# Kernel tuning notes

Measured on AMD Instinct MI355X. Metric: run time of the kernel, lower is better.

## Reference

```python
import jax, jax.numpy as jnp
import numpy as np
from functools import partial

BETA = 0.5
THR = 1.0
NUM_STEPS = 25

@jax.custom_vjp
def spike_fn(x):
    # Heaviside spike; surrogate gradient (snntorch ATan, alpha=2) in bwd.
    return (x > 0).astype(x.dtype)

def _spike_fwd(x):
    return spike_fn(x), x

def _spike_bwd(x, g):
    return (g / (1.0 + (jnp.pi * x) ** 2),)

spike_fn.defvjp(_spike_fwd, _spike_bwd)

def setup_inputs() -> dict:
    key = jax.random.key(0)
    ks = jax.random.split(key, 12)
    B, I, H, O = 16384, 1024, 1024, 10
    s = 0.05
    return {
        "x":   jax.random.normal(ks[0], (B, I), jnp.float32),
        "W1":  jax.random.normal(ks[1], (H, I), jnp.float32) * s,
        "b1":  jax.random.normal(ks[2], (H,), jnp.float32) * s,
        "V1w": jax.random.normal(ks[3], (H, H), jnp.float32) * s,
        "V1b": jax.random.normal(ks[4], (H,), jnp.float32) * s,
        "W2":  jax.random.normal(ks[5], (H, H), jnp.float32) * s,
        "b2":  jax.random.normal(ks[6], (H,), jnp.float32) * s,
        "V2w": jax.random.normal(ks[7], (H, H), jnp.float32) * s,
        "V2b": jax.random.normal(ks[8], (H,), jnp.float32) * s,
        "W3":  jax.random.normal(ks[9], (O, H), jnp.float32) * s,
        "b3":  jax.random.normal(ks[10], (O,), jnp.float32) * s,
    }

def reference(x, W1, b1, V1w, V1b, W2, b2, V2w, V2b, W3, b3):
    B = x.shape[0]
    H = W1.shape[0]
    cur1 = x @ W1.T + b1  # loop-invariant: fc1(x) recomputed identically each step

    def step(carry, _):
        spk1, mem1, spk2, mem2, ssum = carry
        # RLeaky layer 1: soft reset based on previous mem, recurrent linear on prev spikes
        reset1 = (mem1 > THR).astype(mem1.dtype)
        mem1 = BETA * mem1 + cur1 + spk1 @ V1w.T + V1b - reset1 * THR
        spk1 = spike_fn(mem1 - THR)
        cur2 = spk1 @ W2.T + b2
        reset2 = (mem2 > THR).astype(mem2.dtype)
        mem2 = BETA * mem2 + cur2 + spk2 @ V2w.T + V2b - reset2 * THR
        spk2 = spike_fn(mem2 - THR)
        return (spk1, mem1, spk2, mem2, ssum + spk2), None

    z = jnp.zeros((B, H), x.dtype)
    init = (z, z, z, z, z)
    (s1, m1, s2, m2, spk_sum), _ = jax.lax.scan(step, init, None, length=NUM_STEPS)
    return (spk_sum / NUM_STEPS) @ W3.T + b3
```

## Files before the change

### kernel.cpp

```cpp
#include <hip/hip_runtime.h>


#pragma clang fp contract(off)

#define HDIM 1024
#define SPB (HDIM / 8)
#define BATCH 16384
#define NSTEP 25
#define BMR 128
#define BNC 64
#define BK 32
#define NKT (HDIM / BK)
#define KC 512

__device__ __forceinline__ void stage_a_f32(const float* __restrict__ g, float* s,
                                            int tid, int kt) {
  int row = tid & 127, c = tid >> 7;
  const float* src = g + (size_t)row * HDIM + kt * BK + c * 16;
  float4 v0 = *(const float4*)(src);
  float4 v1 = *(const float4*)(src + 4);
  float4 v2 = *(const float4*)(src + 8);
  float4 v3 = *(const float4*)(src + 12);
  int k0 = c * 16;
  s[(k0 + 0) * BMR + row] = v0.x;  s[(k0 + 1) * BMR + row] = v0.y;
  s[(k0 + 2) * BMR + row] = v0.z;  s[(k0 + 3) * BMR + row] = v0.w;
  s[(k0 + 4) * BMR + row] = v1.x;  s[(k0 + 5) * BMR + row] = v1.y;
  s[(k0 + 6) * BMR + row] = v1.z;  s[(k0 + 7) * BMR + row] = v1.w;
  s[(k0 + 8) * BMR + row] = v2.x;  s[(k0 + 9) * BMR + row] = v2.y;
  s[(k0 + 10) * BMR + row] = v2.z; s[(k0 + 11) * BMR + row] = v2.w;
  s[(k0 + 12) * BMR + row] = v3.x; s[(k0 + 13) * BMR + row] = v3.y;
  s[(k0 + 14) * BMR + row] = v3.z; s[(k0 + 15) * BMR + row] = v3.w;
}

__device__ __forceinline__ void stage_a_u1(const unsigned char* __restrict__ g, float* s,
                                           int tid, int kt) {
  int row = tid & 127, c = tid >> 7;
  unsigned short v =
      *(const unsigned short*)(g + (size_t)row * SPB + kt * 4 + c * 2);
  int k0 = c * 16;
#pragma unroll
  for (int q = 0; q < 16; ++q)
    s[(k0 + q) * BMR + row] = (float)((v >> q) & 1u);
}

__device__ __forceinline__ void stage_b(const float* __restrict__ g, float* s,
                                        int tid, int kt) {
  int row = tid & 63, c = tid >> 6;
  const float* src = g + (size_t)row * HDIM + kt * BK + c * 8;
  float4 v0 = *(const float4*)(src);
  float4 v1 = *(const float4*)(src + 4);
  int k0 = c * 8;
  s[(k0 + 0) * BNC + row] = v0.x; s[(k0 + 1) * BNC + row] = v0.y;
  s[(k0 + 2) * BNC + row] = v0.z; s[(k0 + 3) * BNC + row] = v0.w;
  s[(k0 + 4) * BNC + row] = v1.x; s[(k0 + 5) * BNC + row] = v1.y;
  s[(k0 + 6) * BNC + row] = v1.z; s[(k0 + 7) * BNC + row] = v1.w;
}

template <bool AU1>
__device__ __forceinline__ void kpass(const void* __restrict__ Ag,
                                      const float* __restrict__ Bg,
                                      float* sA, float* sB, int tid, int m0, int n0,
                                      float csum[4][8]) {
  float p[4][8];
#pragma unroll
  for (int m = 0; m < 4; ++m)
#pragma unroll
    for (int n = 0; n < 8; ++n) { csum[m][n] = 0.0f; p[m][n] = 0.0f; }

#pragma unroll 1
  for (int kt = 0; kt < NKT; ++kt) {
    if (AU1) stage_a_u1((const unsigned char*)Ag, sA, tid, kt);
    else     stage_a_f32((const float*)Ag, sA, tid, kt);
    stage_b(Bg, sB, tid, kt);
    __syncthreads();
#pragma unroll
    for (int k = 0; k < BK; ++k) {
      float a[4], b[8];
      *(float4*)&a[0] = *(const float4*)&sA[k * BMR + m0];
      *(float4*)&b[0] = *(const float4*)&sB[k * BNC + n0];
      *(float4*)&b[4] = *(const float4*)&sB[k * BNC + n0 + 4];
#pragma unroll
      for (int m = 0; m < 4; ++m)
#pragma unroll
        for (int n = 0; n < 8; ++n)
          p[m][n] = __builtin_fmaf(a[m], b[n], p[m][n]);
    }
    if (((kt + 1) * BK) % KC == 0) {
#pragma unroll
      for (int m = 0; m < 4; ++m)
#pragma unroll
        for (int n = 0; n < 8; ++n) { csum[m][n] = csum[m][n] + p[m][n]; p[m][n] = 0.0f; }
    }
    __syncthreads();
  }
}

__global__ __launch_bounds__(256) void gemm_cur(const float* __restrict__ A,
                                                const float* __restrict__ B,
                                                const float* __restrict__ bias,
                                                float* __restrict__ outv) {
  __shared__ float sA[BK * BMR];
  __shared__ float sB[BK * BNC];
  const int tid = threadIdx.x;
  const int m0 = (tid >> 3) * 4, n0 = (tid & 7) * 8;
  const int bm = blockIdx.y, bn = blockIdx.x;
  float csum[4][8];
  kpass<false>(A + (size_t)bm * BMR * HDIM, B + (size_t)bn * BNC * HDIM,
               sA, sB, tid, m0, n0, csum);
  const int colb = bn * BNC + n0;
  float4 bia0 = *(const float4*)&bias[colb];
  float4 bia1 = *(const float4*)&bias[colb + 4];
  const float bi[8] = {bia0.x, bia0.y, bia0.z, bia0.w, bia1.x, bia1.y, bia1.z, bia1.w};
#pragma unroll
  for (int m = 0; m < 4; ++m) {
    size_t idx = (size_t)(bm * BMR + m0 + m) * HDIM + colb;
    float o[8];
#pragma unroll
    for (int n = 0; n < 8; ++n) o[n] = csum[m][n] + bi[n];
    *(float4*)&outv[idx] = *(float4*)&o[0];
    *(float4*)&outv[idx + 4] = *(float4*)&o[4];
  }
}

__global__ __launch_bounds__(256) void l1_t0(const float* __restrict__ cur1,
                                             const float* __restrict__ vb,
                                             float* __restrict__ memv,
                                             unsigned char* __restrict__ spk_out) {
  size_t i = ((size_t)blockIdx.x * 256 + threadIdx.x) * 8;
  int col = (int)(i & (HDIM - 1));
  size_t row = i >> 10;
  float au[8], tn[8];
  *(float4*)&au[0] = *(const float4*)&cur1[i];
  *(float4*)&au[4] = *(const float4*)&cur1[i + 4];
  float4 v0 = *(const float4*)&vb[col];
  float4 v1 = *(const float4*)&vb[col + 4];
  const float vbv[8] = {v0.x, v0.y, v0.z, v0.w, v1.x, v1.y, v1.z, v1.w};
  unsigned int bits = 0;
#pragma unroll
  for (int n = 0; n < 8; ++n) {
    float t = 0.5f * 0.0f;
    t = t + au[n];
    t = t + 0.0f;
    t = t + vbv[n];
    t = t - 0.0f;
    tn[n] = t;
    bits |= (((t - 1.0f) > 0.0f) ? 1u : 0u) << n;
  }
  *(float4*)&memv[i] = *(float4*)&tn[0];
  *(float4*)&memv[i + 4] = *(float4*)&tn[4];
  spk_out[row * SPB + (col >> 3)] = (unsigned char)bits;
}

__global__ __launch_bounds__(256) void gemm_l1(
    const unsigned char* __restrict__ A, const float* __restrict__ B,
    const float* __restrict__ vb, const float* __restrict__ cur1,
    float* __restrict__ memv, unsigned char* __restrict__ spk_out) {
  __shared__ float sA[BK * BMR];
  __shared__ float sB[BK * BNC];
  const int tid = threadIdx.x;
  const int m0 = (tid >> 3) * 4, n0 = (tid & 7) * 8;
  const int bm = blockIdx.y, bn = blockIdx.x;
  float csum[4][8];
  kpass<true>(A + (size_t)bm * BMR * SPB, B + (size_t)bn * BNC * HDIM,
              sA, sB, tid, m0, n0, csum);
  const int colb = bn * BNC + n0;
  float4 v0 = *(const float4*)&vb[colb];
  float4 v1 = *(const float4*)&vb[colb + 4];
  const float vbv[8] = {v0.x, v0.y, v0.z, v0.w, v1.x, v1.y, v1.z, v1.w};
#pragma unroll
  for (int m = 0; m < 4; ++m) {
    size_t row = (size_t)(bm * BMR + m0 + m);
    size_t idx = row * HDIM + colb;
    float mo[8], au[8], tn[8];
    *(float4*)&mo[0] = *(const float4*)&memv[idx];
    *(float4*)&mo[4] = *(const float4*)&memv[idx + 4];
    *(float4*)&au[0] = *(const float4*)&cur1[idx];
    *(float4*)&au[4] = *(const float4*)&cur1[idx + 4];
    unsigned int bits = 0;
#pragma unroll
    for (int n = 0; n < 8; ++n) {
      float reset = (mo[n] > 1.0f) ? 1.0f : 0.0f;
      float t = 0.5f * mo[n];
      t = t + au[n];
      t = t + csum[m][n];
      t = t + vbv[n];
      t = t - reset;
      tn[n] = t;
      bits |= (((t - 1.0f) > 0.0f) ? 1u : 0u) << n;
    }
    *(float4*)&memv[idx] = *(float4*)&tn[0];
    *(float4*)&memv[idx + 4] = *(float4*)&tn[4];
    spk_out[row * SPB + (colb >> 3)] = (unsigned char)bits;
  }
}

__global__ __launch_bounds__(256) void gemm_l2f(
    const unsigned char* __restrict__ A1, const float* __restrict__ B1,
    const unsigned char* __restrict__ A2, const float* __restrict__ B2,
    const float* __restrict__ bias, const float* __restrict__ vb,
    float* __restrict__ memv, unsigned char* __restrict__ spk_out,
    unsigned char* __restrict__ ssum, int skip2) {
  __shared__ float sA[BK * BMR];
  __shared__ float sB[BK * BNC];
  const int tid = threadIdx.x;
  const int m0 = (tid >> 3) * 4, n0 = (tid & 7) * 8;
  const int bm = blockIdx.y, bn = blockIdx.x;
  float dot1[4][8], csum[4][8];
  kpass<true>(A1 + (size_t)bm * BMR * SPB, B1 + (size_t)bn * BNC * HDIM,
              sA, sB, tid, m0, n0, dot1);
  if (skip2) {
#pragma unroll
    for (int m = 0; m < 4; ++m)
#pragma unroll
      for (int n = 0; n < 8; ++n) csum[m][n] = 0.0f;
  } else {
    __syncthreads();
    kpass<true>(A2 + (size_t)bm * BMR * SPB, B2 + (size_t)bn * BNC * HDIM,
                sA, sB, tid, m0, n0, csum);
  }
  const int colb = bn * BNC + n0;
  float4 b0 = *(const float4*)&bias[colb];
  float4 b1v = *(const float4*)&bias[colb + 4];
  const float bi[8] = {b0.x, b0.y, b0.z, b0.w, b1v.x, b1v.y, b1v.z, b1v.w};
  float4 v0 = *(const float4*)&vb[colb];
  float4 v1 = *(const float4*)&vb[colb + 4];
  const float vbv[8] = {v0.x, v0.y, v0.z, v0.w, v1.x, v1.y, v1.z, v1.w};
#pragma unroll
  for (int m = 0; m < 4; ++m) {
    size_t row = (size_t)(bm * BMR + m0 + m);
    size_t idx = row * HDIM + colb;
    float mo[8], tn[8];
    *(float4*)&mo[0] = *(const float4*)&memv[idx];
    *(float4*)&mo[4] = *(const float4*)&memv[idx + 4];
    unsigned int bits = 0;
#pragma unroll
    for (int n = 0; n < 8; ++n) {
      float reset = (mo[n] > 1.0f) ? 1.0f : 0.0f;
      float cur2 = dot1[m][n] + bi[n];
      float t = 0.5f * mo[n];
      t = t + cur2;
      t = t + csum[m][n];
      t = t + vbv[n];
      t = t - reset;
      tn[n] = t;
      bits |= (((t - 1.0f) > 0.0f) ? 1u : 0u) << n;
    }
    *(float4*)&memv[idx] = *(float4*)&tn[0];
    *(float4*)&memv[idx + 4] = *(float4*)&tn[4];
    spk_out[row * SPB + (colb >> 3)] = (unsigned char)bits;
    unsigned long long old = *(unsigned long long*)&ssum[idx];
    unsigned long long ns = 0;
#pragma unroll
    for (int n = 0; n < 8; ++n) {
      unsigned char c = (unsigned char)(((old >> (8 * n)) & 0xFF) + ((bits >> n) & 1u));
      ns |= ((unsigned long long)c) << (8 * n);
    }
    *(unsigned long long*)&ssum[idx] = ns;
  }
}

__global__ __launch_bounds__(256) void out_blas(const unsigned char* __restrict__ ssum,
                                                const float* __restrict__ W3,
                                                const float* __restrict__ b3,
                                                float* __restrict__ out) {
  int t = blockIdx.x * 256 + threadIdx.x;
  int b = t >> 4, o = t & 15;
  if (o >= 10) return;
  const unsigned char* sp = ssum + (size_t)b * HDIM;
  const float* wp = W3 + (size_t)o * HDIM;
  float csum = 0.0f, p = 0.0f;
#pragma unroll 4
  for (int k = 0; k < HDIM; ++k) {
    float sv = (float)sp[k] / 25.0f;
    p = __builtin_fmaf(sv, wp[k], p);
    if ((k + 1) % KC == 0) { csum = csum + p; p = 0.0f; }
  }
  out[(size_t)b * 10 + o] = csum + b3[o];
}

extern "C" void kernel_launch(void* const* d_in, const int* in_sizes, int n_in,
                              void* d_out, int out_size, void* d_ws, size_t ws_size,
                              hipStream_t stream) {
  const float* x = (const float*)d_in[0];
  const float* W1 = (const float*)d_in[1];
  const float* b1 = (const float*)d_in[2];
  const float* V1w = (const float*)d_in[3];
  const float* V1b = (const float*)d_in[4];
  const float* W2 = (const float*)d_in[5];
  const float* b2 = (const float*)d_in[6];
  const float* V2w = (const float*)d_in[7];
  const float* V2b = (const float*)d_in[8];
  const float* W3 = (const float*)d_in[9];
  const float* b3 = (const float*)d_in[10];
  float* out = (float*)d_out;

  char* ws = (char*)d_ws;
  const size_t per_row = (size_t)HDIM * 4 * 3 + 4 * SPB + (size_t)HDIM;
  size_t rows = BATCH;
  while (rows > 128 && rows * per_row > ws_size) rows >>= 1;
  const int nchunk = (int)(BATCH / rows);
  const size_t RH = rows * (size_t)HDIM;
  const size_t RS = rows * (size_t)SPB;

  size_t off = 0;
  float* cur1 = (float*)(ws + off); off += RH * 4;
  float* mem1 = (float*)(ws + off); off += RH * 4;
  float* mem2 = (float*)(ws + off); off += RH * 4;
  unsigned char *spk1[2], *spk2[2];
  spk1[0] = (unsigned char*)(ws + off); off += RS;
  spk1[1] = (unsigned char*)(ws + off); off += RS;
  spk2[0] = (unsigned char*)(ws + off); off += RS;
  spk2[1] = (unsigned char*)(ws + off); off += RS;
  unsigned char* ssum = (unsigned char*)(ws + off); off += RH;

  dim3 grid(HDIM / BNC, (unsigned)(rows / BMR));

  for (int c = 0; c < nchunk; ++c) {
    const float* xc = x + (size_t)c * RH;
    float* outc = out + (size_t)c * rows * 10;

    hipMemsetAsync(mem2, 0, RH * 4, stream);
    hipMemsetAsync(ssum, 0, RH, stream);

    gemm_cur<<<grid, 256, 0, stream>>>(xc, W1, b1, cur1);

    for (int t = 0; t < NSTEP; ++t) {
      int rd = t & 1, wr = rd ^ 1;
      if (t == 0) {
        l1_t0<<<(unsigned)(RH / (256 * 8)), 256, 0, stream>>>(cur1, V1b, mem1, spk1[wr]);
      } else {
        gemm_l1<<<grid, 256, 0, stream>>>(spk1[rd], V1w, V1b, cur1, mem1, spk1[wr]);
      }
      gemm_l2f<<<grid, 256, 0, stream>>>(spk1[wr], W2, spk2[rd], V2w, b2, V2b,
                                         mem2, spk2[wr], ssum, t == 0 ? 1 : 0);
    }
    out_blas<<<(unsigned)(rows * 16 / 256), 256, 0, stream>>>(ssum, W3, b3, outc);
  }
}
```

Measured before the change: 28.80 ms.

## Read spike bits directly into registers and double-buffer weight tile in LDS

The spike-input GEMMs no longer expand packed bits into a float tile in shared memory. Each thread loads 32-bit words of its own rows' spike bits straight from global memory and extracts each bit as a 0/1 float inside the inner loop. The weight tile is double-buffered with a register prefetch of the next k-tile, which removes one barrier per iteration and overlaps global loads with compute. In exchange there are more uncoalesced per-row global loads, a shift and convert per FMA row, and more register pressure.

```diff
diff --git a/kernel.cpp b/kernel.cpp
--- a/kernel.cpp
+++ b/kernel.cpp
@@ -32,46 +32,100 @@
   s[(k0 + 14) * BMR + row] = v3.z; s[(k0 + 15) * BMR + row] = v3.w;
 }
 
-__device__ __forceinline__ void stage_a_u1(const unsigned char* __restrict__ g, float* s,
-                                           int tid, int kt) {
-  int row = tid & 127, c = tid >> 7;
-  unsigned short v =
-      *(const unsigned short*)(g + (size_t)row * SPB + kt * 4 + c * 2);
-  int k0 = c * 16;
-#pragma unroll
-  for (int q = 0; q < 16; ++q)
-    s[(k0 + q) * BMR + row] = (float)((v >> q) & 1u);
-}
-
-__device__ __forceinline__ void stage_b(const float* __restrict__ g, float* s,
-                                        int tid, int kt) {
+__device__ __forceinline__ void load_b(const float* __restrict__ g, int tid,
+                                       int kt, float r[8]) {
   int row = tid & 63, c = tid >> 6;
   const float* src = g + (size_t)row * HDIM + kt * BK + c * 8;
-  float4 v0 = *(const float4*)(src);
-  float4 v1 = *(const float4*)(src + 4);
-  int k0 = c * 8;
-  s[(k0 + 0) * BNC + row] = v0.x; s[(k0 + 1) * BNC + row] = v0.y;
-  s[(k0 + 2) * BNC + row] = v0.z; s[(k0 + 3) * BNC + row] = v0.w;
-  s[(k0 + 4) * BNC + row] = v1.x; s[(k0 + 5) * BNC + row] = v1.y;
-  s[(k0 + 6) * BNC + row] = v1.z; s[(k0 + 7) * BNC + row] = v1.w;
-}
-
-template <bool AU1>
-__device__ __forceinline__ void kpass(const void* __restrict__ Ag,
-                                      const float* __restrict__ Bg,
-                                      float* sA, float* sB, int tid, int m0, int n0,
-                                      float csum[4][8]) {
+  *(float4*)&r[0] = *(const float4*)(src);
+  *(float4*)&r[4] = *(const float4*)(src + 4);
+}
+
+__device__ __forceinline__ void write_b(float* sB, int tid, const float r[8]) {
+  int row = tid & 63, k0 = (tid >> 6) * 8;
+#pragma unroll
+  for (int q = 0; q < 8; ++q) sB[(k0 + q) * BNC + row] = r[q];
+}
+
+__device__ __forceinline__ void kpass_bits(const unsigned char* __restrict__ Ag,
+                                           const float* __restrict__ Bg,
+                                           float* sB0, float* sB1,
+                                           int tid, int m0, int n0,
+                                           float csum[4][8]) {
   float p[4][8];
 #pragma unroll
   for (int m = 0; m < 4; ++m)
 #pragma unroll
     for (int n = 0; n < 8; ++n) { csum[m][n] = 0.0f; p[m][n] = 0.0f; }
+
+  const unsigned char* ar[4];
+#pragma unroll
+  for (int m = 0; m < 4; ++m) ar[m] = Ag + (size_t)(m0 + m) * SPB;
+
+  float rb[8];
+  unsigned int awc[4];
+  load_b(Bg, tid, 0, rb);
+#pragma unroll
+  for (int m = 0; m < 4; ++m) awc[m] = *(const unsigned int*)(ar[m]);
+  write_b(sB0, tid, rb);
+  __syncthreads();
 
 #pragma unroll 1
   for (int kt = 0; kt < NKT; ++kt) {
-    if (AU1) stage_a_u1((const unsigned char*)Ag, sA, tid, kt);
-    else     stage_a_f32((const float*)Ag, sA, tid, kt);
-    stage_b(Bg, sB, tid, kt);
+    float* cB = (kt & 1) ? sB1 : sB0;
+    float* nB = (kt & 1) ? sB0 : sB1;
+    float rbn[8];
+    unsigned int awn[4];
+    if (kt + 1 < NKT) {
+      load_b(Bg, tid, kt + 1, rbn);
+#pragma unroll
+      for (int m = 0; m < 4; ++m)
+        awn[m] = *(const unsigned int*)(ar[m] + (kt + 1) * 4);
+    }
+#pragma unroll
+    for (int k = 0; k < BK; ++k) {
+      float b[8];
+      *(float4*)&b[0] = *(const float4*)&cB[k * BNC + n0];
+      *(float4*)&b[4] = *(const float4*)&cB[k * BNC + n0 + 4];
+      float a[4];
+#pragma unroll
+      for (int m = 0; m < 4; ++m) a[m] = (float)((awc[m] >> k) & 1u);
+#pragma unroll
+      for (int m = 0; m < 4; ++m)
+#pragma unroll
+        for (int n = 0; n < 8; ++n)
+          p[m][n] = __builtin_fmaf(a[m], b[n], p[m][n]);
+    }
+    if (((kt + 1) * BK) % KC == 0) {
+#pragma unroll
+      for (int m = 0; m < 4; ++m)
+#pragma unroll
+        for (int n = 0; n < 8; ++n) { csum[m][n] = csum[m][n] + p[m][n]; p[m][n] = 0.0f; }
+    }
+    if (kt + 1 < NKT) {
+      write_b(nB, tid, rbn);
+#pragma unroll
+      for (int m = 0; m < 4; ++m) awc[m] = awn[m];
+    }
+    __syncthreads();
+  }
+}
+
+__device__ __forceinline__ void kpass_f32(const float* __restrict__ Ag,
+                                          const float* __restrict__ Bg,
+                                          float* sA, float* sB, int tid,
+                                          int m0, int n0, float csum[4][8]) {
+  float p[4][8];
+#pragma unroll
+  for (int m = 0; m < 4; ++m)
+#pragma unroll
+    for (int n = 0; n < 8; ++n) { csum[m][n] = 0.0f; p[m][n] = 0.0f; }
+
+#pragma unroll 1
+  for (int kt = 0; kt < NKT; ++kt) {
+    stage_a_f32(Ag, sA, tid, kt);
+    float rb[8];
+    load_b(Bg, tid, kt, rb);
+    write_b(sB, tid, rb);
     __syncthreads();
 #pragma unroll
     for (int k = 0; k < BK; ++k) {
@@ -105,8 +159,8 @@
   const int m0 = (tid >> 3) * 4, n0 = (tid & 7) * 8;
   const int bm = blockIdx.y, bn = blockIdx.x;
   float csum[4][8];
-  kpass<false>(A + (size_t)bm * BMR * HDIM, B + (size_t)bn * BNC * HDIM,
-               sA, sB, tid, m0, n0, csum);
+  kpass_f32(A + (size_t)bm * BMR * HDIM, B + (size_t)bn * BNC * HDIM,
+            sA, sB, tid, m0, n0, csum);
   const int colb = bn * BNC + n0;
   float4 bia0 = *(const float4*)&bias[colb];
   float4 bia1 = *(const float4*)&bias[colb + 4];
@@ -155,14 +209,14 @@
     const unsigned char* __restrict__ A, const float* __restrict__ B,
     const float* __restrict__ vb, const float* __restrict__ cur1,
     float* __restrict__ memv, unsigned char* __restrict__ spk_out) {
-  __shared__ float sA[BK * BMR];
-  __shared__ float sB[BK * BNC];
+  __shared__ float sB0[BK * BNC];
+  __shared__ float sB1[BK * BNC];
   const int tid = threadIdx.x;
   const int m0 = (tid >> 3) * 4, n0 = (tid & 7) * 8;
   const int bm = blockIdx.y, bn = blockIdx.x;
   float csum[4][8];
-  kpass<true>(A + (size_t)bm * BMR * SPB, B + (size_t)bn * BNC * HDIM,
-              sA, sB, tid, m0, n0, csum);
+  kpass_bits(A + (size_t)bm * BMR * SPB, B + (size_t)bn * BNC * HDIM,
+             sB0, sB1, tid, m0, n0, csum);
   const int colb = bn * BNC + n0;
   float4 v0 = *(const float4*)&vb[colb];
   float4 v1 = *(const float4*)&vb[colb + 4];
@@ -200,23 +254,22 @@
     const float* __restrict__ bias, const float* __restrict__ vb,
     float* __restrict__ memv, unsigned char* __restrict__ spk_out,
     unsigned char* __restrict__ ssum, int skip2) {
-  __shared__ float sA[BK * BMR];
-  __shared__ float sB[BK * BNC];
+  __shared__ float sB0[BK * BNC];
+  __shared__ float sB1[BK * BNC];
   const int tid = threadIdx.x;
   const int m0 = (tid >> 3) * 4, n0 = (tid & 7) * 8;
   const int bm = blockIdx.y, bn = blockIdx.x;
   float dot1[4][8], csum[4][8];
-  kpass<true>(A1 + (size_t)bm * BMR * SPB, B1 + (size_t)bn * BNC * HDIM,
-              sA, sB, tid, m0, n0, dot1);
+  kpass_bits(A1 + (size_t)bm * BMR * SPB, B1 + (size_t)bn * BNC * HDIM,
+             sB0, sB1, tid, m0, n0, dot1);
   if (skip2) {
 #pragma unroll
     for (int m = 0; m < 4; ++m)
 #pragma unroll
       for (int n = 0; n < 8; ++n) csum[m][n] = 0.0f;
   } else {
-    __syncthreads();
-    kpass<true>(A2 + (size_t)bm * BMR * SPB, B2 + (size_t)bn * BNC * HDIM,
-                sA, sB, tid, m0, n0, csum);
+    kpass_bits(A2 + (size_t)bm * BMR * SPB, B2 + (size_t)bn * BNC * HDIM,
+               sB0, sB1, tid, m0, n0, csum);
   }
   const int colb = bn * BNC + n0;
   float4 b0 = *(const float4*)&bias[colb];
```

After: 40.00 ms. 1.39x slower.
